# Kernel tuning notes

Hardware: AMD Instinct MI355X
Metric: run time of the kernel (lower is better)

The kernel has to match this reference:

```python
import jax, jax.numpy as jnp
import numpy as np

D_IN = 1024
D_OUT = 1024
B, S = 4, 4096


def setup_inputs() -> dict:
    key = jax.random.key(0)
    ks = jax.random.split(key, 7)
    scale = 1.0 / np.sqrt(D_IN)
    return {
        "x": jax.random.normal(ks[0], (B, S, D_IN), dtype=jnp.float32),
        "Wq": jax.random.uniform(ks[1], (D_IN, D_OUT), jnp.float32, -scale, scale),
        "bq": jax.random.uniform(ks[2], (D_OUT,), jnp.float32, -scale, scale),
        "Wk": jax.random.uniform(ks[3], (D_IN, D_OUT), jnp.float32, -scale, scale),
        "bk": jax.random.uniform(ks[4], (D_OUT,), jnp.float32, -scale, scale),
        "Wv": jax.random.uniform(ks[5], (D_IN, D_OUT), jnp.float32, -scale, scale),
        "bv": jax.random.uniform(ks[6], (D_OUT,), jnp.float32, -scale, scale),
    }


def reference(x, Wq, bq, Wk, bk, Wv, bv):
    # x: [B,S,d_in]
    q = jnp.einsum("bsd,de->bse", x, Wq) + bq  # [B,S,d_out]
    k = jnp.einsum("bsd,de->bse", x, Wk) + bk
    v = jnp.einsum("bsd,de->bse", x, Wv) + bv
    scores = jnp.einsum("bqe,bke->bqk", q, k) / jnp.sqrt(jnp.float32(D_OUT))  # [B,S,S]
    attn = jax.nn.softmax(scores, axis=2)
    return jnp.einsum("bqk,bke->bqe", attn, v)  # [B,S,d_out]
```

## Files before the change

### kernel.cpp

```cpp
#include <hip/hip_runtime.h>
#include <cstdint>

#define SEQ 4096
#define NB 4
#define DIM 1024
#define MTOT (NB * SEQ)

using u16x8  = __attribute__((ext_vector_type(8))) unsigned short;
using bf16x8 = __attribute__((ext_vector_type(8))) __bf16;
using f32x4  = __attribute__((ext_vector_type(4))) float;

__device__ __forceinline__ unsigned short f2bf(float f) {
  unsigned u = __builtin_bit_cast(unsigned, f);
  u += 0x7fffu + ((u >> 16) & 1u);
  return (unsigned short)(u >> 16);
}
__device__ __forceinline__ float bf2f(unsigned short h) {
  return __builtin_bit_cast(float, (unsigned)h << 16);
}

__device__ __forceinline__ void gload16(const unsigned short* g, unsigned short* l) {
  __builtin_amdgcn_global_load_lds(
      (const __attribute__((address_space(1))) unsigned int*)g,
      (__attribute__((address_space(3))) unsigned int*)l, 16, 0, 0);
}

__device__ __forceinline__ void stage_half(const unsigned short* gsrc, size_t ld,
                                           unsigned short* ldst) {
  gload16(gsrc, ldst);
  gload16(gsrc + 64 * ld, ldst + 64 * 64);
}

#define BAR()   __builtin_amdgcn_s_barrier()
#define FENCE() asm volatile("" ::: "memory")

__global__ __launch_bounds__(256) void cvt_x(const float* __restrict__ in,
                                             unsigned short* __restrict__ out) {
  size_t i = ((size_t)blockIdx.x * 256 + threadIdx.x) * 4;
  float4 v = *(const float4*)(in + i);
  ushort4 o;
  o.x = f2bf(v.x); o.y = f2bf(v.y); o.z = f2bf(v.z); o.w = f2bf(v.w);
  *(ushort4*)(out + i) = o;
}

__global__ __launch_bounds__(256) void transpose_w(const float* __restrict__ W,
                                                   unsigned short* __restrict__ WT) {
  __shared__ float tile[32][33];
  const int tx = threadIdx.x, ty = threadIdx.y;
  const int d0 = blockIdx.y * 32, e0 = blockIdx.x * 32;
#pragma unroll
  for (int j = 0; j < 32; j += 8)
    tile[ty + j][tx] = W[(size_t)(d0 + ty + j) * DIM + e0 + tx];
  __syncthreads();
#pragma unroll
  for (int j = 0; j < 32; j += 8)
    WT[(size_t)(e0 + ty + j) * DIM + d0 + tx] = f2bf(tile[tx][ty + j]);
}

enum { EPI_QK = 0, EPI_VT = 1, EPI_EXP = 2, EPI_F32DIV = 3 };

template <int EPI>
__global__ __launch_bounds__(512, 2) void gemm256(
    const unsigned short* __restrict__ A, long sA,
    const unsigned short* __restrict__ B, long sB,
    void* __restrict__ C, long sC,
    const float* __restrict__ bias,
    float* __restrict__ lsum,
    int K, int lda, int ldb, int ldc, float scale) {
  __shared__ unsigned short sm[2][2][256 * 64];
  const int t    = threadIdx.x;
  const int lane = t & 63;
  const int wave = t >> 6;
  const int wm   = wave >> 2;
  const int wn   = wave & 3;
  const int fr   = lane & 15;
  const int g    = lane >> 4;
  const int xr   = (fr & 7) << 4;

  const size_t row0 = (size_t)blockIdx.x * 256;
  const size_t col0 = (size_t)blockIdx.y * 256;
  const unsigned short* Ab = A + (size_t)blockIdx.z * (size_t)sA;
  const unsigned short* Bb = B + (size_t)blockIdx.z * (size_t)sB;

  const int srow = t >> 3;
  const int scol = ((((t & 7) << 4) ^ ((srow & 7) << 4)) >> 1);
  const unsigned short* gA = Ab + (row0 + srow) * (size_t)lda + scol;
  const unsigned short* gB = Bb + (col0 + srow) * (size_t)ldb + scol;

  const int arow = wm * 128 + fr;
  const int brow = wn * 64 + fr;
  const int c0 = (((g << 4)) ^ xr) >> 1;
  const int c1 = ((64 | (g << 4)) ^ xr) >> 1;

  f32x4 acc[8][4];
  const f32x4 z4 = {0.f, 0.f, 0.f, 0.f};
#pragma unroll
  for (int i = 0; i < 8; ++i)
#pragma unroll
    for (int j = 0; j < 4; ++j) acc[i][j] = z4;

  const int nt = K >> 6;

  stage_half(gA, lda, &sm[0][0][wave * 512]);
  stage_half(gA + 128 * (size_t)lda, lda, &sm[0][0][8192 + wave * 512]);
  stage_half(gB, ldb, &sm[0][1][wave * 512]);
  stage_half(gB + 128 * (size_t)ldb, ldb, &sm[0][1][8192 + wave * 512]);
  if (nt > 1) {
    stage_half(gB + 64, ldb, &sm[1][1][wave * 512]);
    stage_half(gB + 128 * (size_t)ldb + 64, ldb, &sm[1][1][8192 + wave * 512]);
    stage_half(gA + 64, lda, &sm[1][0][wave * 512]);
    asm volatile("s_waitcnt vmcnt(6)" ::: "memory");
  } else {
    asm volatile("s_waitcnt vmcnt(0)" ::: "memory");
  }
  BAR(); FENCE();

  bf16x8 a0[4][2], a1[4][2], b0[2][2], b1[2][2];

  for (int kt = 0; kt < nt; ++kt) {
    const int p = kt & 1;
    const unsigned short* As  = sm[p][0];
    const unsigned short* Bs2 = sm[p][1];

#pragma unroll
    for (int mi = 0; mi < 4; ++mi) {
      a0[mi][0] = *(const bf16x8*)(As + (arow + mi * 16) * 64 + c0);
      a0[mi][1] = *(const bf16x8*)(As + (arow + mi * 16) * 64 + c1);
    }
#pragma unroll
    for (int ni = 0; ni < 2; ++ni) {
      b0[ni][0] = *(const bf16x8*)(Bs2 + (brow + ni * 16) * 64 + c0);
      b0[ni][1] = *(const bf16x8*)(Bs2 + (brow + ni * 16) * 64 + c1);
    }
    if (kt + 1 < nt)
      stage_half(gA + 128 * (size_t)lda + (size_t)(kt + 1) * 64, lda,
                 &sm[p ^ 1][0][8192 + wave * 512]);
    FENCE(); BAR(); FENCE();
    __builtin_amdgcn_s_setprio(1);
#pragma unroll
    for (int mi = 0; mi < 4; ++mi)
#pragma unroll
      for (int ni = 0; ni < 2; ++ni) {
        acc[mi][ni] = __builtin_amdgcn_mfma_f32_16x16x32_bf16(a0[mi][0], b0[ni][0], acc[mi][ni], 0, 0, 0);
        acc[mi][ni] = __builtin_amdgcn_mfma_f32_16x16x32_bf16(a0[mi][1], b0[ni][1], acc[mi][ni], 0, 0, 0);
      }
    __builtin_amdgcn_s_setprio(0);
    FENCE(); BAR(); FENCE();

#pragma unroll
    for (int ni = 0; ni < 2; ++ni) {
      b1[ni][0] = *(const bf16x8*)(Bs2 + (brow + (ni + 2) * 16) * 64 + c0);
      b1[ni][1] = *(const bf16x8*)(Bs2 + (brow + (ni + 2) * 16) * 64 + c1);
    }
    FENCE(); BAR(); FENCE();
    __builtin_amdgcn_s_setprio(1);
#pragma unroll
    for (int mi = 0; mi < 4; ++mi)
#pragma unroll
      for (int ni = 0; ni < 2; ++ni) {
        acc[mi][ni + 2] = __builtin_amdgcn_mfma_f32_16x16x32_bf16(a0[mi][0], b1[ni][0], acc[mi][ni + 2], 0, 0, 0);
        acc[mi][ni + 2] = __builtin_amdgcn_mfma_f32_16x16x32_bf16(a0[mi][1], b1[ni][1], acc[mi][ni + 2], 0, 0, 0);
      }
    __builtin_amdgcn_s_setprio(0);
    FENCE(); BAR(); FENCE();

#pragma unroll
    for (int mi = 0; mi < 4; ++mi) {
      a1[mi][0] = *(const bf16x8*)(As + (arow + (mi + 4) * 16) * 64 + c0);
      a1[mi][1] = *(const bf16x8*)(As + (arow + (mi + 4) * 16) * 64 + c1);
    }
    if (kt + 2 < nt)
      stage_half(gB + (size_t)(kt + 2) * 64, ldb, &sm[p][1][wave * 512]);
    FENCE(); BAR(); FENCE();
    __builtin_amdgcn_s_setprio(1);
#pragma unroll
    for (int mi = 0; mi < 4; ++mi)
#pragma unroll
      for (int ni = 0; ni < 2; ++ni) {
        acc[mi + 4][ni] = __builtin_amdgcn_mfma_f32_16x16x32_bf16(a1[mi][0], b0[ni][0], acc[mi + 4][ni], 0, 0, 0);
        acc[mi + 4][ni] = __builtin_amdgcn_mfma_f32_16x16x32_bf16(a1[mi][1], b0[ni][1], acc[mi + 4][ni], 0, 0, 0);
      }
    __builtin_amdgcn_s_setprio(0);
    FENCE(); BAR(); FENCE();

    if (kt + 2 < nt) {
      stage_half(gB + 128 * (size_t)ldb + (size_t)(kt + 2) * 64, ldb,
                 &sm[p][1][8192 + wave * 512]);
      stage_half(gA + (size_t)(kt + 2) * 64, lda, &sm[p][0][wave * 512]);
      asm volatile("s_waitcnt vmcnt(6)" ::: "memory");
    } else {
      asm volatile("s_waitcnt vmcnt(0)" ::: "memory");
    }
    FENCE(); BAR(); FENCE();
    __builtin_amdgcn_s_setprio(1);
#pragma unroll
    for (int mi = 0; mi < 4; ++mi)
#pragma unroll
      for (int ni = 0; ni < 2; ++ni) {
        acc[mi + 4][ni + 2] = __builtin_amdgcn_mfma_f32_16x16x32_bf16(a1[mi][0], b1[ni][0], acc[mi + 4][ni + 2], 0, 0, 0);
        acc[mi + 4][ni + 2] = __builtin_amdgcn_mfma_f32_16x16x32_bf16(a1[mi][1], b1[ni][1], acc[mi + 4][ni + 2], 0, 0, 0);
      }
    __builtin_amdgcn_s_setprio(0);
    FENCE(); BAR(); FENCE();
  }

  char* Lb = (char*)&sm[0][0][0];
  const int rb = (lane >> 4) * 4;

  if constexpr (EPI == EPI_QK || EPI == EPI_EXP) {
    float bb[4];
    if constexpr (EPI == EPI_QK) {
#pragma unroll
      for (int ni = 0; ni < 4; ++ni) bb[ni] = bias[col0 + wn * 64 + ni * 16 + fr];
    }
#pragma unroll
    for (int mi = 0; mi < 8; ++mi) {
      const int r0 = wm * 128 + mi * 16 + rb;
#pragma unroll
      for (int ni = 0; ni < 4; ++ni) {
        const int c = wn * 64 + ni * 16 + fr;
#pragma unroll
        for (int j = 0; j < 4; ++j) {
          const int r = r0 + j;
          float v = acc[mi][ni][j];
          if constexpr (EPI == EPI_EXP) v = __expf(v * scale);
          else                          v = v + bb[ni];
          *(unsigned short*)(Lb + r * 512 + ((c * 2) ^ ((r & 7) << 4))) = f2bf(v);
        }
      }
    }
    __syncthreads();
    unsigned short* Co = (unsigned short*)C +
        (EPI == EPI_EXP ? (size_t)blockIdx.z * (size_t)sC : (size_t)0);
#pragma unroll 4
    for (int i = 0; i < 16; ++i) {
      const int G = i * 512 + t;
      const int r = G >> 5, c16 = G & 31;
      u16x8 v = *(const u16x8*)(Lb + r * 512 + ((c16 * 16) ^ ((r & 7) << 4)));
      *(u16x8*)(Co + (row0 + r) * (size_t)ldc + col0 + c16 * 8) = v;
    }
    if constexpr (EPI == EPI_EXP) {
      const int r = t >> 1;
      float s = 0.f;
#pragma unroll
      for (int k = 0; k < 16; ++k) {
        const int c16 = (t & 1) * 16 + k;
        u16x8 v = *(const u16x8*)(Lb + r * 512 + ((c16 * 16) ^ ((r & 7) << 4)));
#pragma unroll
        for (int q = 0; q < 8; ++q) s += bf2f(v[q]);
      }
      atomicAdd(&lsum[(size_t)blockIdx.z * SEQ + row0 + r], s);
    }
  } else if constexpr (EPI == EPI_VT) {
#pragma unroll
    for (int ni = 0; ni < 4; ++ni) {
      const int c = wn * 64 + ni * 16 + fr;
      const float bb = bias[col0 + c];
#pragma unroll
      for (int mi = 0; mi < 8; ++mi) {
        const int r0 = wm * 128 + mi * 16 + rb;
        ushort4 pk;
        pk.x = f2bf(acc[mi][ni][0] + bb);
        pk.y = f2bf(acc[mi][ni][1] + bb);
        pk.z = f2bf(acc[mi][ni][2] + bb);
        pk.w = f2bf(acc[mi][ni][3] + bb);
        *(ushort4*)(Lb + c * 512 + ((r0 * 2) ^ ((c & 7) << 4))) = pk;
      }
    }
    __syncthreads();
    unsigned short* Co = (unsigned short*)C;
#pragma unroll 4
    for (int i = 0; i < 16; ++i) {
      const int G = i * 512 + t;
      const int e = G >> 5, m16 = G & 31;
      u16x8 v = *(const u16x8*)(Lb + e * 512 + ((m16 * 16) ^ ((e & 7) << 4)));
      *(u16x8*)(Co + (col0 + e) * (size_t)ldc + row0 + m16 * 8) = v;
    }
  } else {
    float* Co = (float*)C + (size_t)blockIdx.z * (size_t)sC;
#pragma unroll
    for (int h = 0; h < 2; ++h) {
      if (h) __syncthreads();
      if (wm == h) {
#pragma unroll
        for (int mi = 0; mi < 8; ++mi) {
          const int r0 = mi * 16 + rb;
#pragma unroll
          for (int ni = 0; ni < 4; ++ni) {
            const int c = wn * 64 + ni * 16 + fr;
#pragma unroll
            for (int j = 0; j < 4; ++j) {
              const int r = r0 + j;
              *(float*)(Lb + r * 1024 + ((c * 4) ^ ((r & 7) << 4))) = acc[mi][ni][j];
            }
          }
        }
      }
      __syncthreads();
#pragma unroll 4
      for (int i = 0; i < 16; ++i) {
        const int G = i * 512 + t;
        const int r = G >> 6, c4 = G & 63;
        f32x4 v = *(const f32x4*)(Lb + r * 1024 + ((c4 * 16) ^ ((r & 7) << 4)));
        const size_t grow = row0 + h * 128 + r;
        const float inv = 1.0f / lsum[(size_t)blockIdx.z * SEQ + grow];
        v *= inv;
        *(f32x4*)(Co + grow * (size_t)ldc + col0 + c4 * 4) = v;
      }
    }
  }
}

extern "C" void kernel_launch(void* const* d_in, const int* in_sizes, int n_in,
                              void* d_out, int out_size, void* d_ws, size_t ws_size,
                              hipStream_t stream) {
  (void)in_sizes; (void)n_in; (void)out_size;
  const float* x  = (const float*)d_in[0];
  const float* Wq = (const float*)d_in[1];
  const float* bq = (const float*)d_in[2];
  const float* Wk = (const float*)d_in[3];
  const float* bk = (const float*)d_in[4];
  const float* Wv = (const float*)d_in[5];
  const float* bv = (const float*)d_in[6];
  float* out = (float*)d_out;

  const size_t EL   = (size_t)MTOT * DIM;
  const size_t SALL = (size_t)NB * SEQ * SEQ;
  unsigned short* Q  = (unsigned short*)d_ws;
  unsigned short* Km = Q + EL;
  unsigned short* VT = Km + EL;
  unsigned short* Sb = VT + EL;
  unsigned short* WT = Sb + SALL;
  float*          l  = (float*)(WT + (size_t)3 * DIM * DIM);
  unsigned short* xb = Sb;

  hipMemsetAsync(l, 0, MTOT * sizeof(float), stream);

  cvt_x<<<dim3(EL / 1024), dim3(256), 0, stream>>>(x, xb);
  transpose_w<<<dim3(32, 32), dim3(32, 8), 0, stream>>>(Wq, WT);
  transpose_w<<<dim3(32, 32), dim3(32, 8), 0, stream>>>(Wk, WT + DIM * DIM);
  transpose_w<<<dim3(32, 32), dim3(32, 8), 0, stream>>>(Wv, WT + 2 * DIM * DIM);

  dim3 gp(MTOT / 256, DIM / 256, 1);
  gemm256<EPI_QK><<<gp, 512, 0, stream>>>(xb, 0, WT, 0, Q, 0, bq, nullptr,
                                          DIM, DIM, DIM, DIM, 1.f);
  gemm256<EPI_QK><<<gp, 512, 0, stream>>>(xb, 0, WT + DIM * DIM, 0, Km, 0, bk, nullptr,
                                          DIM, DIM, DIM, DIM, 1.f);
  gemm256<EPI_VT><<<gp, 512, 0, stream>>>(xb, 0, WT + 2 * DIM * DIM, 0, VT, 0, bv, nullptr,
                                          DIM, DIM, DIM, MTOT, 1.f);

  const float sc = 0.03125f;
  gemm256<EPI_EXP><<<dim3(SEQ / 256, SEQ / 256, NB), 512, 0, stream>>>(
      Q, (long)SEQ * DIM, Km, (long)SEQ * DIM, Sb, (long)SEQ * SEQ, nullptr, l,
      DIM, DIM, DIM, SEQ, sc);
  gemm256<EPI_F32DIV><<<dim3(SEQ / 256, DIM / 256, NB), 512, 0, stream>>>(
      Sb, (long)SEQ * SEQ, VT, (long)SEQ, out, (long)SEQ * DIM, nullptr, l,
      SEQ, SEQ, MTOT, DIM, 1.f);
}
```

Measured before the change: 419.7 us.

## Fuse QKV projections into one GEMM launch and remap PV block order

Merges the three separate Q, K, V projection GEMMs into a single launch over a concatenated weight matrix, with a concatenated bias buffer built by a small kernel. The epilogue picks Q/K row-major or V transposed output by column block. The exp epilogue switches to exp2f with a log2e-folded scale. The PV GEMM remaps block indices so that blocks sharing data are scheduled together, aiming for better L2 reuse. This removes launch overhead and tail effects at the cost of an extra tiny kernel and some epilogue branching.

```diff
diff --git a/kernel.cpp b/kernel.cpp
--- a/kernel.cpp
+++ b/kernel.cpp
@@ -5,6 +5,7 @@
 #define NB 4
 #define DIM 1024
 #define MTOT (NB * SEQ)
+constexpr size_t EL = (size_t)MTOT * DIM;
 
 using u16x8  = __attribute__((ext_vector_type(8))) unsigned short;
 using bf16x8 = __attribute__((ext_vector_type(8))) __bf16;
@@ -24,7 +25,6 @@
       (const __attribute__((address_space(1))) unsigned int*)g,
       (__attribute__((address_space(3))) unsigned int*)l, 16, 0, 0);
 }
-
 __device__ __forceinline__ void stage_half(const unsigned short* gsrc, size_t ld,
                                            unsigned short* ldst) {
   gload16(gsrc, ldst);
@@ -57,16 +57,23 @@
     WT[(size_t)(e0 + ty + j) * DIM + d0 + tx] = f2bf(tile[tx][ty + j]);
 }
 
-enum { EPI_QK = 0, EPI_VT = 1, EPI_EXP = 2, EPI_F32DIV = 3 };
+__global__ __launch_bounds__(256) void cat_bias(const float* __restrict__ bq,
+                                                const float* __restrict__ bk,
+                                                const float* __restrict__ bv,
+                                                float* __restrict__ bcat) {
+  int i = blockIdx.x * 256 + threadIdx.x;
+  float v = (i < 1024) ? bq[i] : (i < 2048) ? bk[i - 1024] : bv[i - 2048];
+  bcat[i] = v;
+}
+
+enum { EPI_QKV = 0, EPI_EXP = 1, EPI_PV = 2 };
 
 template <int EPI>
-__global__ __launch_bounds__(512, 2) void gemm256(
-    const unsigned short* __restrict__ A, long sA,
-    const unsigned short* __restrict__ B, long sB,
-    void* __restrict__ C, long sC,
-    const float* __restrict__ bias,
-    float* __restrict__ lsum,
-    int K, int lda, int ldb, int ldc, float scale) {
+__device__ __forceinline__ void gemm_body(
+    const unsigned short* __restrict__ A, const unsigned short* __restrict__ B,
+    void* __restrict__ C, const float* __restrict__ bias, float* __restrict__ lsum,
+    int K, int lda, int ldb, int ldc, float scale,
+    int row0, int col0, int bz, long sA, long sB, long sC) {
   __shared__ unsigned short sm[2][2][256 * 64];
   const int t    = threadIdx.x;
   const int lane = t & 63;
@@ -77,15 +84,13 @@
   const int g    = lane >> 4;
   const int xr   = (fr & 7) << 4;
 
-  const size_t row0 = (size_t)blockIdx.x * 256;
-  const size_t col0 = (size_t)blockIdx.y * 256;
-  const unsigned short* Ab = A + (size_t)blockIdx.z * (size_t)sA;
-  const unsigned short* Bb = B + (size_t)blockIdx.z * (size_t)sB;
+  const unsigned short* Ab = A + (size_t)bz * (size_t)sA;
+  const unsigned short* Bb = B + (size_t)bz * (size_t)sB;
 
   const int srow = t >> 3;
   const int scol = ((((t & 7) << 4) ^ ((srow & 7) << 4)) >> 1);
-  const unsigned short* gA = Ab + (row0 + srow) * (size_t)lda + scol;
-  const unsigned short* gB = Bb + (col0 + srow) * (size_t)ldb + scol;
+  const unsigned short* gA = Ab + (size_t)(row0 + srow) * (size_t)lda + scol;
+  const unsigned short* gB = Bb + (size_t)(col0 + srow) * (size_t)ldb + scol;
 
   const int arow = wm * 128 + fr;
   const int brow = wn * 64 + fr;
@@ -207,12 +212,62 @@
   char* Lb = (char*)&sm[0][0][0];
   const int rb = (lane >> 4) * 4;
 
-  if constexpr (EPI == EPI_QK || EPI == EPI_EXP) {
-    float bb[4];
-    if constexpr (EPI == EPI_QK) {
+  if constexpr (EPI == EPI_QKV) {
+    const int which = col0 >> 10;
+    const int lc0   = col0 & 1023;
+    unsigned short* Co = (unsigned short*)C + (size_t)which * EL;
+    if (which < 2) {
+      float bb[4];
 #pragma unroll
       for (int ni = 0; ni < 4; ++ni) bb[ni] = bias[col0 + wn * 64 + ni * 16 + fr];
-    }
+#pragma unroll
+      for (int mi = 0; mi < 8; ++mi) {
+        const int r0 = wm * 128 + mi * 16 + rb;
+#pragma unroll
+        for (int ni = 0; ni < 4; ++ni) {
+          const int c = wn * 64 + ni * 16 + fr;
+#pragma unroll
+          for (int j = 0; j < 4; ++j) {
+            const int r = r0 + j;
+            *(unsigned short*)(Lb + r * 512 + ((c * 2) ^ ((r & 7) << 4))) =
+                f2bf(acc[mi][ni][j] + bb[ni]);
+          }
+        }
+      }
+      __syncthreads();
+#pragma unroll 4
+      for (int i = 0; i < 16; ++i) {
+        const int G = i * 512 + t;
+        const int r = G >> 5, c16 = G & 31;
+        u16x8 v = *(const u16x8*)(Lb + r * 512 + ((c16 * 16) ^ ((r & 7) << 4)));
+        *(u16x8*)(Co + (size_t)(row0 + r) * DIM + lc0 + c16 * 8) = v;
+      }
+    } else {
+#pragma unroll
+      for (int ni = 0; ni < 4; ++ni) {
+        const int c = wn * 64 + ni * 16 + fr;
+        const float bb = bias[col0 + c];
+#pragma unroll
+        for (int mi = 0; mi < 8; ++mi) {
+          const int r0 = wm * 128 + mi * 16 + rb;
+          ushort4 pk;
+          pk.x = f2bf(acc[mi][ni][0] + bb);
+          pk.y = f2bf(acc[mi][ni][1] + bb);
+          pk.z = f2bf(acc[mi][ni][2] + bb);
+          pk.w = f2bf(acc[mi][ni][3] + bb);
+          *(ushort4*)(Lb + c * 512 + ((r0 * 2) ^ ((c & 7) << 4))) = pk;
+        }
+      }
+      __syncthreads();
+#pragma unroll 4
+      for (int i = 0; i < 16; ++i) {
+        const int G = i * 512 + t;
+        const int e = G >> 5, m16 = G & 31;
+        u16x8 v = *(const u16x8*)(Lb + e * 512 + ((m16 * 16) ^ ((e & 7) << 4)));
+        *(u16x8*)(Co + (size_t)(lc0 + e) * MTOT + row0 + m16 * 8) = v;
+      }
+    }
+  } else if constexpr (EPI == EPI_EXP) {
 #pragma unroll
     for (int mi = 0; mi < 8; ++mi) {
       const int r0 = wm * 128 + mi * 16 + rb;
@@ -222,24 +277,21 @@
 #pragma unroll
         for (int j = 0; j < 4; ++j) {
           const int r = r0 + j;
-          float v = acc[mi][ni][j];
-          if constexpr (EPI == EPI_EXP) v = __expf(v * scale);
-          else                          v = v + bb[ni];
-          *(unsigned short*)(Lb + r * 512 + ((c * 2) ^ ((r & 7) << 4))) = f2bf(v);
+          *(unsigned short*)(Lb + r * 512 + ((c * 2) ^ ((r & 7) << 4))) =
+              f2bf(exp2f(acc[mi][ni][j] * scale));
         }
       }
     }
     __syncthreads();
-    unsigned short* Co = (unsigned short*)C +
-        (EPI == EPI_EXP ? (size_t)blockIdx.z * (size_t)sC : (size_t)0);
+    unsigned short* Co = (unsigned short*)C + (size_t)bz * (size_t)sC;
 #pragma unroll 4
     for (int i = 0; i < 16; ++i) {
       const int G = i * 512 + t;
       const int r = G >> 5, c16 = G & 31;
       u16x8 v = *(const u16x8*)(Lb + r * 512 + ((c16 * 16) ^ ((r & 7) << 4)));
-      *(u16x8*)(Co + (row0 + r) * (size_t)ldc + col0 + c16 * 8) = v;
-    }
-    if constexpr (EPI == EPI_EXP) {
+      *(u16x8*)(Co + (size_t)(row0 + r) * (size_t)ldc + col0 + c16 * 8) = v;
+    }
+    {
       const int r = t >> 1;
       float s = 0.f;
 #pragma unroll
@@ -249,35 +301,10 @@
 #pragma unroll
         for (int q = 0; q < 8; ++q) s += bf2f(v[q]);
       }
-      atomicAdd(&lsum[(size_t)blockIdx.z * SEQ + row0 + r], s);
-    }
-  } else if constexpr (EPI == EPI_VT) {
-#pragma unroll
-    for (int ni = 0; ni < 4; ++ni) {
-      const int c = wn * 64 + ni * 16 + fr;
-      const float bb = bias[col0 + c];
-#pragma unroll
-      for (int mi = 0; mi < 8; ++mi) {
-        const int r0 = wm * 128 + mi * 16 + rb;
-        ushort4 pk;
-        pk.x = f2bf(acc[mi][ni][0] + bb);
-        pk.y = f2bf(acc[mi][ni][1] + bb);
-        pk.z = f2bf(acc[mi][ni][2] + bb);
-        pk.w = f2bf(acc[mi][ni][3] + bb);
-        *(ushort4*)(Lb + c * 512 + ((r0 * 2) ^ ((c & 7) << 4))) = pk;
-      }
-    }
-    __syncthreads();
-    unsigned short* Co = (unsigned short*)C;
-#pragma unroll 4
-    for (int i = 0; i < 16; ++i) {
-      const int G = i * 512 + t;
-      const int e = G >> 5, m16 = G & 31;
-      u16x8 v = *(const u16x8*)(Lb + e * 512 + ((m16 * 16) ^ ((e & 7) << 4)));
-      *(u16x8*)(Co + (col0 + e) * (size_t)ldc + row0 + m16 * 8) = v;
+      atomicAdd(&lsum[(size_t)bz * SEQ + row0 + r], s);
     }
   } else {
-    float* Co = (float*)C + (size_t)blockIdx.z * (size_t)sC;
+    float* Co = (float*)C + (size_t)bz * (size_t)sC;
 #pragma unroll
     for (int h = 0; h < 2; ++h) {
       if (h) __syncthreads();
@@ -302,19 +329,48 @@
         const int G = i * 512 + t;
         const int r = G >> 6, c4 = G & 63;
         f32x4 v = *(const f32x4*)(Lb + r * 1024 + ((c4 * 16) ^ ((r & 7) << 4)));
-        const size_t grow = row0 + h * 128 + r;
-        const float inv = 1.0f / lsum[(size_t)blockIdx.z * SEQ + grow];
+        const size_t grow = (size_t)row0 + h * 128 + r;
+        const float inv = 1.0f / lsum[(size_t)bz * SEQ + grow];
         v *= inv;
         *(f32x4*)(Co + grow * (size_t)ldc + col0 + c4 * 4) = v;
       }
     }
   }
+}
+
+__global__ __launch_bounds__(512, 2) void gemm_qkv(
+    const unsigned short* __restrict__ A, const unsigned short* __restrict__ B,
+    unsigned short* __restrict__ C, const float* __restrict__ bcat) {
+  gemm_body<EPI_QKV>(A, B, C, bcat, nullptr, DIM, DIM, DIM, DIM, 1.f,
+                     (int)blockIdx.x * 256, (int)blockIdx.y * 256, 0, 0, 0, 0);
+}
+
+__global__ __launch_bounds__(512, 2) void gemm_exp(
+    const unsigned short* __restrict__ A, const unsigned short* __restrict__ B,
+    unsigned short* __restrict__ C, float* __restrict__ lsum) {
+  gemm_body<EPI_EXP>(A, B, C, nullptr, lsum, DIM, DIM, DIM, SEQ, 0.04508422f,
+                     (int)blockIdx.x * 256, (int)blockIdx.y * 256, (int)blockIdx.z,
+                     (long)SEQ * DIM, (long)SEQ * DIM, (long)SEQ * SEQ);
+}
+
+__global__ __launch_bounds__(512, 2) void gemm_pv(
+    const unsigned short* __restrict__ A, const unsigned short* __restrict__ B,
+    float* __restrict__ C, float* __restrict__ lsum) {
+  const int flat = (int)blockIdx.x +
+                   (int)gridDim.x * ((int)blockIdx.y + (int)gridDim.y * (int)blockIdx.z);
+  const int nf  = (flat & 7) * 32 + (flat >> 3);
+  const int b   = nf >> 6;
+  const int rc  = nf & 63;
+  const int row = rc >> 2, col = rc & 3;
+  gemm_body<EPI_PV>(A, B, C, nullptr, lsum, SEQ, SEQ, MTOT, DIM, 1.f,
+                    row * 256, col * 256, b,
+                    (long)SEQ * SEQ, (long)SEQ, (long)SEQ * DIM);
 }
 
 extern "C" void kernel_launch(void* const* d_in, const int* in_sizes, int n_in,
                               void* d_out, int out_size, void* d_ws, size_t ws_size,
                               hipStream_t stream) {
-  (void)in_sizes; (void)n_in; (void)out_size;
+  (void)in_sizes; (void)n_in; (void)out_size; (void)ws_size;
   const float* x  = (const float*)d_in[0];
   const float* Wq = (const float*)d_in[1];
   const float* bq = (const float*)d_in[2];
@@ -324,7 +380,6 @@
   const float* bv = (const float*)d_in[6];
   float* out = (float*)d_out;
 
-  const size_t EL   = (size_t)MTOT * DIM;
   const size_t SALL = (size_t)NB * SEQ * SEQ;
   unsigned short* Q  = (unsigned short*)d_ws;
   unsigned short* Km = Q + EL;
@@ -332,6 +387,7 @@
   unsigned short* Sb = VT + EL;
   unsigned short* WT = Sb + SALL;
   float*          l  = (float*)(WT + (size_t)3 * DIM * DIM);
+  float*          bc = l + MTOT;
   unsigned short* xb = Sb;
 
   hipMemsetAsync(l, 0, MTOT * sizeof(float), stream);
@@ -340,20 +396,11 @@
   transpose_w<<<dim3(32, 32), dim3(32, 8), 0, stream>>>(Wq, WT);
   transpose_w<<<dim3(32, 32), dim3(32, 8), 0, stream>>>(Wk, WT + DIM * DIM);
   transpose_w<<<dim3(32, 32), dim3(32, 8), 0, stream>>>(Wv, WT + 2 * DIM * DIM);
-
-  dim3 gp(MTOT / 256, DIM / 256, 1);
-  gemm256<EPI_QK><<<gp, 512, 0, stream>>>(xb, 0, WT, 0, Q, 0, bq, nullptr,
-                                          DIM, DIM, DIM, DIM, 1.f);
-  gemm256<EPI_QK><<<gp, 512, 0, stream>>>(xb, 0, WT + DIM * DIM, 0, Km, 0, bk, nullptr,
-                                          DIM, DIM, DIM, DIM, 1.f);
-  gemm256<EPI_VT><<<gp, 512, 0, stream>>>(xb, 0, WT + 2 * DIM * DIM, 0, VT, 0, bv, nullptr,
-                                          DIM, DIM, DIM, MTOT, 1.f);
-
-  const float sc = 0.03125f;
-  gemm256<EPI_EXP><<<dim3(SEQ / 256, SEQ / 256, NB), 512, 0, stream>>>(
-      Q, (long)SEQ * DIM, Km, (long)SEQ * DIM, Sb, (long)SEQ * SEQ, nullptr, l,
-      DIM, DIM, DIM, SEQ, sc);
-  gemm256<EPI_F32DIV><<<dim3(SEQ / 256, DIM / 256, NB), 512, 0, stream>>>(
-      Sb, (long)SEQ * SEQ, VT, (long)SEQ, out, (long)SEQ * DIM, nullptr, l,
-      SEQ, SEQ, MTOT, DIM, 1.f);
-}
+  cat_bias<<<dim3(12), dim3(256), 0, stream>>>(bq, bk, bv, bc);
+
+  gemm_qkv<<<dim3(MTOT / 256, 3 * DIM / 256), 512, 0, stream>>>(xb, WT, Q, bc);
+
+  gemm_exp<<<dim3(SEQ / 256, SEQ / 256, NB), 512, 0, stream>>>(Q, Km, Sb, l);
+
+  gemm_pv<<<dim3(DIM / 256, SEQ / 256, NB), 512, 0, stream>>>(Sb, VT, out, l);
+}
```

After: 412.9 us. No clear change (-1.6%).
